# Kernel tuning notes

Measured on AMD Instinct MI355X. Metric: run time of the kernel, lower is better.

Reference implementation:

```python
import jax, jax.numpy as jnp
import numpy as np

B, N, E = 4, 50000, 800000
C_IN, C_OUT, EF, EH = 64, 64, 10, 4  # heads=1, concat=False


def setup_inputs() -> dict:
    key = jax.random.key(0)
    ks = jax.random.split(key, 11)
    x = jax.random.normal(ks[0], (B, N, C_IN), jnp.float32)
    edge_index = jax.random.randint(ks[1], (2, E), 0, N, jnp.int32)
    edge_attr = jax.random.normal(ks[2], (E, EF), jnp.float32)
    # edge MLP params (both Linear layers bias=False)
    W1 = jax.random.normal(ks[3], (EF, EH), jnp.float32) / np.sqrt(EF)
    W2 = jax.random.normal(ks[4], (EH, EH), jnp.float32) / np.sqrt(EH)
    # GATConv params (heads=1): shared lin for src/dst, edge lin, attention vectors, bias
    W = jax.random.normal(ks[5], (C_IN, C_OUT), jnp.float32) / np.sqrt(C_IN)
    lin_edge_W = jax.random.normal(ks[6], (EH, C_OUT), jnp.float32) / np.sqrt(EH)
    att_src = jax.random.normal(ks[7], (C_OUT,), jnp.float32) / np.sqrt(C_OUT)
    att_dst = jax.random.normal(ks[8], (C_OUT,), jnp.float32) / np.sqrt(C_OUT)
    att_edge = jax.random.normal(ks[9], (C_OUT,), jnp.float32) / np.sqrt(C_OUT)
    bias = jnp.zeros((C_OUT,), jnp.float32)
    return {"x": x, "edge_index": edge_index, "edge_attr": edge_attr,
            "W1": W1, "W2": W2, "W": W, "lin_edge_W": lin_edge_W,
            "att_src": att_src, "att_dst": att_dst, "att_edge": att_edge,
            "bias": bias}


def reference(x, edge_index, edge_attr, W1, W2, W, lin_edge_W,
              att_src, att_dst, att_edge, bias):
    # edge MLP (LeakyReLU default slope 0.01), batch-independent
    e = jax.nn.leaky_relu(edge_attr @ W1, 0.01) @ W2            # [E, EH]
    src, dst = edge_index[0], edge_index[1]
    # PyG GATConv default add_self_loops=True, fill_value='mean':
    # self-loop edge attr = mean of incoming edge attrs per dst node
    cnt = jax.ops.segment_sum(jnp.ones((E,), e.dtype), dst, num_segments=N)
    loop_attr = jax.ops.segment_sum(e, dst, num_segments=N) / jnp.maximum(cnt, 1.0)[:, None]
    e_full = jnp.concatenate([e, loop_attr], axis=0)            # [E+N, EH]
    ar = jnp.arange(N, dtype=src.dtype)
    src_f = jnp.concatenate([src, ar])
    dst_f = jnp.concatenate([dst, ar])
    # edge attention logit contribution (batch-independent)
    a_edge = (e_full @ lin_edge_W) @ att_edge                   # [E+N]

    def per_batch(xb):
        h = xb @ W                                              # [N, C_OUT]
        a_s = h @ att_src                                       # [N]
        a_d = h @ att_dst                                       # [N]
        logits = jax.nn.leaky_relu(a_s[src_f] + a_d[dst_f] + a_edge, 0.2)
        # segment softmax over incoming edges of each dst node
        m = jax.ops.segment_max(logits, dst_f, num_segments=N)
        ex = jnp.exp(logits - m[dst_f])
        denom = jax.ops.segment_sum(ex, dst_f, num_segments=N)
        alpha = ex / denom[dst_f]                               # [E+N]
        out = jax.ops.segment_sum(h[src_f] * alpha[:, None], dst_f, num_segments=N)
        return jax.nn.elu(out + bias)                           # [N, C_OUT]

    # vectorizes the original Python loop over the batch dim
    return jax.vmap(per_batch)(x)  # dropout p=0.5 is identity in eval mode
```

## Files before the change

kernel.cpp:

```cpp
#include <hip/hip_runtime.h>
#include <math.h>

#define NN 50000
#define NE 800000
#define NB 4
#define C  64
#define EF 10
#define EH 4

__device__ __forceinline__ float lrelu(float x, float s) { return x > 0.f ? x : s * x; }

__device__ __forceinline__ unsigned int f2bf(float f) {
    unsigned u = __float_as_uint(f);
    u += 0x7FFF + ((u >> 16) & 1);
    return u >> 16;
}

__global__ void __launch_bounds__(256) fused_prep_kernel(
        const float* __restrict__ x, const float* __restrict__ W,
        const float* __restrict__ att_src, const float* __restrict__ att_dst,
        unsigned* __restrict__ hbf, float* __restrict__ a_s, float* __restrict__ a_d,
        const float* __restrict__ edge_attr, const int* __restrict__ edge_index,
        const float* __restrict__ W1, const float* __restrict__ W2,
        const float* __restrict__ linW, const float* __restrict__ attE,
        int* __restrict__ cnt, int* __restrict__ rank, float* __restrict__ aE) {
    __shared__ float Wl[C * C];
    __shared__ float xT[C * 64];
    __shared__ float u4s[EH];
    int t = threadIdx.x;
    int bid = blockIdx.x;

    if ((bid & 1) == 0) {
        if (t < 64) {
            float av = attE[t];
            float vv[EH];
#pragma unroll
            for (int h = 0; h < EH; h++) {
                float p = linW[h * C + t] * av;
#pragma unroll
                for (int off = 32; off; off >>= 1) p += __shfl_xor(p, off);
                vv[h] = p;
            }
            if (t < EH) {
                float s = 0.f;
#pragma unroll
                for (int h = 0; h < EH; h++) s += W2[t * EH + h] * vv[h];
                u4s[t] = s;
            }
        }
        int e = (bid >> 1) * 256 + t;
        int d = edge_index[NE + e];
        rank[e] = atomicAdd(&cnt[d], 1);
        const float* ea = edge_attr + (size_t)e * EF;
        float s0 = 0.f, s1 = 0.f, s2 = 0.f, s3 = 0.f;
#pragma unroll
        for (int f = 0; f < EF; f++) {
            float ev = ea[f];
            s0 += ev * W1[f * EH + 0];
            s1 += ev * W1[f * EH + 1];
            s2 += ev * W1[f * EH + 2];
            s3 += ev * W1[f * EH + 3];
        }
        __syncthreads();
        aE[e] = lrelu(s0, 0.01f) * u4s[0] + lrelu(s1, 0.01f) * u4s[1] +
                lrelu(s2, 0.01f) * u4s[2] + lrelu(s3, 0.01f) * u4s[3];
        return;
    }

    for (int i = t * 4; i < C * C; i += 256 * 4)
        *(float4*)&Wl[i] = *(const float4*)&W[i];
    size_t row0 = (size_t)(bid >> 1) * 64;
    int r = t >> 2;
    int k0 = (t & 3) * 16;
    const float4* xr = (const float4*)(x + (row0 + r) * C + k0);
    float4 v0 = xr[0], v1 = xr[1], v2 = xr[2], v3 = xr[3];
    xT[(k0 + 0) * 64 + r] = v0.x;  xT[(k0 + 1) * 64 + r] = v0.y;
    xT[(k0 + 2) * 64 + r] = v0.z;  xT[(k0 + 3) * 64 + r] = v0.w;
    xT[(k0 + 4) * 64 + r] = v1.x;  xT[(k0 + 5) * 64 + r] = v1.y;
    xT[(k0 + 6) * 64 + r] = v1.z;  xT[(k0 + 7) * 64 + r] = v1.w;
    xT[(k0 + 8) * 64 + r] = v2.x;  xT[(k0 + 9) * 64 + r] = v2.y;
    xT[(k0 + 10) * 64 + r] = v2.z; xT[(k0 + 11) * 64 + r] = v2.w;
    xT[(k0 + 12) * 64 + r] = v3.x; xT[(k0 + 13) * 64 + r] = v3.y;
    xT[(k0 + 14) * 64 + r] = v3.z; xT[(k0 + 15) * 64 + r] = v3.w;
    __syncthreads();

    int col4 = (t & 15) * 4;
    int row4 = (t >> 4) * 4;
    float acc[4][4];
#pragma unroll
    for (int i = 0; i < 4; i++)
#pragma unroll
        for (int j = 0; j < 4; j++) acc[i][j] = 0.f;

#pragma unroll 8
    for (int k = 0; k < C; k++) {
        float4 wv = *(float4*)&Wl[k * C + col4];
        float4 xv = *(float4*)&xT[k * 64 + row4];
        const float xs[4] = {xv.x, xv.y, xv.z, xv.w};
        const float ws[4] = {wv.x, wv.y, wv.z, wv.w};
#pragma unroll
        for (int i = 0; i < 4; i++)
#pragma unroll
            for (int j = 0; j < 4; j++) acc[i][j] += xs[i] * ws[j];
    }

#pragma unroll
    for (int i = 0; i < 4; i++) {
        size_t gr = row0 + row4 + i;
        int b = (int)(gr / NN);
        int n = (int)(gr - (size_t)b * NN);
        uint2 p;
        p.x = f2bf(acc[i][0]) | (f2bf(acc[i][1]) << 16);
        p.y = f2bf(acc[i][2]) | (f2bf(acc[i][3]) << 16);
        *(uint2*)&hbf[((size_t)n * NB + b) * (C / 2) + (col4 >> 1)] = p;
    }
    float4 sa = *(const float4*)&att_src[col4];
    float4 da = *(const float4*)&att_dst[col4];
#pragma unroll
    for (int i = 0; i < 4; i++) {
        float ps = acc[i][0] * sa.x + acc[i][1] * sa.y + acc[i][2] * sa.z + acc[i][3] * sa.w;
        float pd = acc[i][0] * da.x + acc[i][1] * da.y + acc[i][2] * da.z + acc[i][3] * da.w;
#pragma unroll
        for (int off = 8; off; off >>= 1) {
            ps += __shfl_xor(ps, off);
            pd += __shfl_xor(pd, off);
        }
        if ((t & 15) == 0) {
            a_s[row0 + row4 + i] = ps;
            a_d[row0 + row4 + i] = pd;
        }
    }
}

__global__ void scan_block_kernel(const int* __restrict__ cnt, int* __restrict__ rowptr,
                                  int* __restrict__ bsum) {
    __shared__ int sh[1024];
    int i = blockIdx.x * 1024 + threadIdx.x;
    sh[threadIdx.x] = (i < NN) ? cnt[i] : 0;
    __syncthreads();
    for (int off = 1; off < 1024; off <<= 1) {
        int t = (threadIdx.x >= (unsigned)off) ? sh[threadIdx.x - off] : 0;
        __syncthreads();
        sh[threadIdx.x] += t;
        __syncthreads();
    }
    if (i < NN) rowptr[1 + i] = sh[threadIdx.x];
    if (threadIdx.x == 1023) bsum[blockIdx.x] = sh[1023];
}

__global__ void scan_add_kernel(int* __restrict__ rowptr, const int* __restrict__ bsum) {
    __shared__ int sbase;
    int bid = blockIdx.x;
    if (threadIdx.x < 64) {
        int v = (threadIdx.x < bid) ? bsum[threadIdx.x] : 0;
#pragma unroll
        for (int off = 32; off; off >>= 1) v += __shfl_xor(v, off);
        if (threadIdx.x == 0) sbase = v;
    }
    __syncthreads();
    int i = bid * 1024 + threadIdx.x;
    if (i < NN) rowptr[1 + i] += sbase;
    if (i == 0) rowptr[0] = 0;
}

__global__ void scatter_kernel(const int* __restrict__ edge_index,
                               const int* __restrict__ rowptr,
                               const int* __restrict__ rank,
                               const float* __restrict__ aE,
                               uint2* __restrict__ csr) {
    int g0 = blockIdx.x * blockDim.x + threadIdx.x;
    if (g0 >= NE / 4) return;
#pragma unroll
    for (int q = 0; q < 4; q++) {
        int e = g0 + q * (NE / 4);
        int s = edge_index[e];
        int d = edge_index[NE + e];
        int idx = rowptr[d] + rank[e];
        uint2 p;
        p.x = (unsigned)s;
        p.y = __float_as_uint(aE[e]);
        csr[idx] = p;
    }
}

__global__ void gather_kernel(const int* __restrict__ rowptr, const uint2* __restrict__ csr,
                              const float* __restrict__ a_s, const float* __restrict__ a_d,
                              const uint2* __restrict__ hbf,
                              const float* __restrict__ bias, float* __restrict__ out) {
    int n = blockIdx.x * (blockDim.x >> 6) + (threadIdx.x >> 6);
    if (n >= NN) return;
    int lane = threadIdx.x & 63;
    int b = lane >> 4;
    int t = lane & 15;
    int r0 = rowptr[n];
    int deg = rowptr[n + 1] - r0;
    const float* asb = a_s + (size_t)b * NN;
    float adst = a_d[(size_t)b * NN + n];

    float ds = 0.f;
    float aEs = 0.f;
    float4 acc = make_float4(0.f, 0.f, 0.f, 0.f);
    for (int base = 0; base < deg; base += 16) {
        int j = base + t;
        float ex = 0.f;
        int sreg = 0;
        if (j < deg) {
            uint2 pr = csr[r0 + j];
            sreg = (int)pr.x;
            float aev = __uint_as_float(pr.y);
            aEs += aev;
            ex = __expf(lrelu(asb[sreg] + adst + aev, 0.2f));
        }
        ds += ex;
        int cn = min(16, deg - base);
        for (int jo = 0; jo < cn; jo += 8) {
            float al[8];
            uint2 hv[8];
#pragma unroll
            for (int k2 = 0; k2 < 8; k2++) {
                int j2 = jo + k2;
                int sl = (b << 4) + (j2 & 15);
                float av = __shfl(ex, sl);
                int sj = __shfl(sreg, sl);
                al[k2] = (j2 < cn) ? av : 0.f;
                hv[k2] = hbf[(size_t)sj * (NB * C / 4) + (b << 4) + t];
            }
#pragma unroll
            for (int k2 = 0; k2 < 8; k2++) {
                acc.x += al[k2] * __uint_as_float(hv[k2].x << 16);
                acc.y += al[k2] * __uint_as_float(hv[k2].x & 0xFFFF0000u);
                acc.z += al[k2] * __uint_as_float(hv[k2].y << 16);
                acc.w += al[k2] * __uint_as_float(hv[k2].y & 0xFFFF0000u);
            }
        }
    }
#pragma unroll
    for (int off = 8; off; off >>= 1) {
        ds += __shfl_xor(ds, off);
        aEs += __shfl_xor(aEs, off);
    }
    float a_loop = aEs / fmaxf((float)deg, 1.0f);
    float eloop = __expf(lrelu(asb[n] + adst + a_loop, 0.2f));
    float inv = 1.f / (ds + eloop);
    uint2 hv = hbf[(size_t)n * (NB * C / 4) + (b << 4) + t];
    float4 bv = ((const float4*)bias)[t];
    float4 o;
    o.x = (acc.x + eloop * __uint_as_float(hv.x << 16)) * inv + bv.x;
    o.y = (acc.y + eloop * __uint_as_float(hv.x & 0xFFFF0000u)) * inv + bv.y;
    o.z = (acc.z + eloop * __uint_as_float(hv.y << 16)) * inv + bv.z;
    o.w = (acc.w + eloop * __uint_as_float(hv.y & 0xFFFF0000u)) * inv + bv.w;
    o.x = o.x > 0.f ? o.x : __expf(o.x) - 1.f;
    o.y = o.y > 0.f ? o.y : __expf(o.y) - 1.f;
    o.z = o.z > 0.f ? o.z : __expf(o.z) - 1.f;
    o.w = o.w > 0.f ? o.w : __expf(o.w) - 1.f;
    ((float4*)out)[((size_t)b * NN + n) * 16 + t] = o;
}

extern "C" void kernel_launch(void* const* d_in, const int* in_sizes, int n_in,
                              void* d_out, int out_size, void* d_ws, size_t ws_size,
                              hipStream_t stream) {
    const float* x      = (const float*)d_in[0];
    const int* eidx     = (const int*)d_in[1];
    const float* eattr  = (const float*)d_in[2];
    const float* W1     = (const float*)d_in[3];
    const float* W2     = (const float*)d_in[4];
    const float* W      = (const float*)d_in[5];
    const float* linW   = (const float*)d_in[6];
    const float* attS   = (const float*)d_in[7];
    const float* attD   = (const float*)d_in[8];
    const float* attE   = (const float*)d_in[9];
    const float* bias   = (const float*)d_in[10];
    float* out = (float*)d_out;

    size_t off = 0;
    auto alloc = [&](size_t bytes) {
        void* p = (char*)d_ws + off;
        off += (bytes + 255) / 256 * 256;
        return p;
    };
    int* cnt      = (int*)alloc((size_t)NN * 4);
    int* rowptr   = (int*)alloc((size_t)(NN + 1) * 4);
    int* bsum     = (int*)alloc(64 * 4);
    int* rank     = (int*)alloc((size_t)NE * 4);
    float* aE     = (float*)alloc((size_t)NE * 4);
    uint2* csr    = (uint2*)alloc((size_t)NE * 8);
    unsigned* hbf = (unsigned*)alloc((size_t)NN * NB * C * 2);
    float* a_s    = (float*)alloc((size_t)NB * NN * 4);
    float* a_d    = (float*)alloc((size_t)NB * NN * 4);
    (void)ws_size; (void)n_in; (void)in_sizes; (void)out_size;

    hipMemsetAsync(cnt, 0, (size_t)NN * 4, stream);

    fused_prep_kernel<<<6250, 256, 0, stream>>>(x, W, attS, attD, hbf, a_s, a_d,
                                                eattr, eidx, W1, W2, linW, attE,
                                                cnt, rank, aE);

    int nblk = (NN + 1023) / 1024;
    scan_block_kernel<<<nblk, 1024, 0, stream>>>(cnt, rowptr, bsum);
    scan_add_kernel<<<nblk, 1024, 0, stream>>>(rowptr, bsum);

    scatter_kernel<<<(NE / 4 + 255) / 256, 256, 0, stream>>>(eidx, rowptr, rank, aE, csr);

    gather_kernel<<<(NN + 3) / 4, 256, 0, stream>>>(rowptr, csr, a_s, a_d,
                                                    (const uint2*)hbf, bias, out);
}
```

Before: 150.7 us.

## Move degree counting first and fuse edge MLP with CSR scatter

The atomic degree/rank counting moves into a small standalone kernel that runs before the prefix scan. The edge-MLP computation then happens inside the fused GEMM kernel after the scan, so each edge writes its (src, attention) pair straight to its CSR slot. This removes the separate scatter kernel and the aE intermediate buffer round trip. In exchange the edge index is read twice and there is one extra launch for the degree pass.

```diff
diff --git a/kernel.cpp b/kernel.cpp
--- a/kernel.cpp
+++ b/kernel.cpp
@@ -16,14 +16,52 @@
     return u >> 16;
 }
 
-__global__ void __launch_bounds__(256) fused_prep_kernel(
+__global__ void degree_kernel(const int* __restrict__ edge_index, int* __restrict__ cnt,
+                              int* __restrict__ rank) {
+    int e = blockIdx.x * blockDim.x + threadIdx.x;
+    if (e < NE) rank[e] = atomicAdd(&cnt[edge_index[NE + e]], 1);
+}
+
+__global__ void scan_block_kernel(const int* __restrict__ cnt, int* __restrict__ rowptr,
+                                  int* __restrict__ bsum) {
+    __shared__ int sh[1024];
+    int i = blockIdx.x * 1024 + threadIdx.x;
+    sh[threadIdx.x] = (i < NN) ? cnt[i] : 0;
+    __syncthreads();
+    for (int off = 1; off < 1024; off <<= 1) {
+        int t = (threadIdx.x >= (unsigned)off) ? sh[threadIdx.x - off] : 0;
+        __syncthreads();
+        sh[threadIdx.x] += t;
+        __syncthreads();
+    }
+    if (i < NN) rowptr[1 + i] = sh[threadIdx.x];
+    if (threadIdx.x == 1023) bsum[blockIdx.x] = sh[1023];
+}
+
+__global__ void scan_add_kernel(int* __restrict__ rowptr, const int* __restrict__ bsum) {
+    __shared__ int sbase;
+    int bid = blockIdx.x;
+    if (threadIdx.x < 64) {
+        int v = (threadIdx.x < bid) ? bsum[threadIdx.x] : 0;
+#pragma unroll
+        for (int off = 32; off; off >>= 1) v += __shfl_xor(v, off);
+        if (threadIdx.x == 0) sbase = v;
+    }
+    __syncthreads();
+    int i = bid * 1024 + threadIdx.x;
+    if (i < NN) rowptr[1 + i] += sbase;
+    if (i == 0) rowptr[0] = 0;
+}
+
+__global__ void __launch_bounds__(256) fused_mlp_scatter_gemm_kernel(
         const float* __restrict__ x, const float* __restrict__ W,
         const float* __restrict__ att_src, const float* __restrict__ att_dst,
         unsigned* __restrict__ hbf, float* __restrict__ a_s, float* __restrict__ a_d,
         const float* __restrict__ edge_attr, const int* __restrict__ edge_index,
         const float* __restrict__ W1, const float* __restrict__ W2,
         const float* __restrict__ linW, const float* __restrict__ attE,
-        int* __restrict__ cnt, int* __restrict__ rank, float* __restrict__ aE) {
+        const int* __restrict__ rowptr, const int* __restrict__ rank,
+        uint2* __restrict__ csr) {
     __shared__ float Wl[C * C];
     __shared__ float xT[C * 64];
     __shared__ float u4s[EH];
@@ -49,8 +87,9 @@
             }
         }
         int e = (bid >> 1) * 256 + t;
+        int s = edge_index[e];
         int d = edge_index[NE + e];
-        rank[e] = atomicAdd(&cnt[d], 1);
+        int idx = rowptr[d] + rank[e];
         const float* ea = edge_attr + (size_t)e * EF;
         float s0 = 0.f, s1 = 0.f, s2 = 0.f, s3 = 0.f;
 #pragma unroll
@@ -62,8 +101,12 @@
             s3 += ev * W1[f * EH + 3];
         }
         __syncthreads();
-        aE[e] = lrelu(s0, 0.01f) * u4s[0] + lrelu(s1, 0.01f) * u4s[1] +
-                lrelu(s2, 0.01f) * u4s[2] + lrelu(s3, 0.01f) * u4s[3];
+        float a = lrelu(s0, 0.01f) * u4s[0] + lrelu(s1, 0.01f) * u4s[1] +
+                  lrelu(s2, 0.01f) * u4s[2] + lrelu(s3, 0.01f) * u4s[3];
+        uint2 p;
+        p.x = (unsigned)s;
+        p.y = __float_as_uint(a);
+        csr[idx] = p;
         return;
     }
 
@@ -132,57 +175,6 @@
     }
 }
 
-__global__ void scan_block_kernel(const int* __restrict__ cnt, int* __restrict__ rowptr,
-                                  int* __restrict__ bsum) {
-    __shared__ int sh[1024];
-    int i = blockIdx.x * 1024 + threadIdx.x;
-    sh[threadIdx.x] = (i < NN) ? cnt[i] : 0;
-    __syncthreads();
-    for (int off = 1; off < 1024; off <<= 1) {
-        int t = (threadIdx.x >= (unsigned)off) ? sh[threadIdx.x - off] : 0;
-        __syncthreads();
-        sh[threadIdx.x] += t;
-        __syncthreads();
-    }
-    if (i < NN) rowptr[1 + i] = sh[threadIdx.x];
-    if (threadIdx.x == 1023) bsum[blockIdx.x] = sh[1023];
-}
-
-__global__ void scan_add_kernel(int* __restrict__ rowptr, const int* __restrict__ bsum) {
-    __shared__ int sbase;
-    int bid = blockIdx.x;
-    if (threadIdx.x < 64) {
-        int v = (threadIdx.x < bid) ? bsum[threadIdx.x] : 0;
-#pragma unroll
-        for (int off = 32; off; off >>= 1) v += __shfl_xor(v, off);
-        if (threadIdx.x == 0) sbase = v;
-    }
-    __syncthreads();
-    int i = bid * 1024 + threadIdx.x;
-    if (i < NN) rowptr[1 + i] += sbase;
-    if (i == 0) rowptr[0] = 0;
-}
-
-__global__ void scatter_kernel(const int* __restrict__ edge_index,
-                               const int* __restrict__ rowptr,
-                               const int* __restrict__ rank,
-                               const float* __restrict__ aE,
-                               uint2* __restrict__ csr) {
-    int g0 = blockIdx.x * blockDim.x + threadIdx.x;
-    if (g0 >= NE / 4) return;
-#pragma unroll
-    for (int q = 0; q < 4; q++) {
-        int e = g0 + q * (NE / 4);
-        int s = edge_index[e];
-        int d = edge_index[NE + e];
-        int idx = rowptr[d] + rank[e];
-        uint2 p;
-        p.x = (unsigned)s;
-        p.y = __float_as_uint(aE[e]);
-        csr[idx] = p;
-    }
-}
-
 __global__ void gather_kernel(const int* __restrict__ rowptr, const uint2* __restrict__ csr,
                               const float* __restrict__ a_s, const float* __restrict__ a_d,
                               const uint2* __restrict__ hbf,
@@ -282,7 +274,6 @@
     int* rowptr   = (int*)alloc((size_t)(NN + 1) * 4);
     int* bsum     = (int*)alloc(64 * 4);
     int* rank     = (int*)alloc((size_t)NE * 4);
-    float* aE     = (float*)alloc((size_t)NE * 4);
     uint2* csr    = (uint2*)alloc((size_t)NE * 8);
     unsigned* hbf = (unsigned*)alloc((size_t)NN * NB * C * 2);
     float* a_s    = (float*)alloc((size_t)NB * NN * 4);
@@ -291,15 +282,15 @@
 
     hipMemsetAsync(cnt, 0, (size_t)NN * 4, stream);
 
-    fused_prep_kernel<<<6250, 256, 0, stream>>>(x, W, attS, attD, hbf, a_s, a_d,
-                                                eattr, eidx, W1, W2, linW, attE,
-                                                cnt, rank, aE);
+    degree_kernel<<<(NE + 255) / 256, 256, 0, stream>>>(eidx, cnt, rank);
 
     int nblk = (NN + 1023) / 1024;
     scan_block_kernel<<<nblk, 1024, 0, stream>>>(cnt, rowptr, bsum);
     scan_add_kernel<<<nblk, 1024, 0, stream>>>(rowptr, bsum);
 
-    scatter_kernel<<<(NE / 4 + 255) / 256, 256, 0, stream>>>(eidx, rowptr, rank, aE, csr);
+    fused_mlp_scatter_gemm_kernel<<<6250, 256, 0, stream>>>(
+        x, W, attS, attD, hbf, a_s, a_d,
+        eattr, eidx, W1, W2, linW, attE, rowptr, rank, csr);
 
     gather_kernel<<<(NN + 3) / 4, 256, 0, stream>>>(rowptr, csr, a_s, a_d,
                                                     (const uint2*)hbf, bias, out);
```

New measurement: 171.8 us. 1.14x slower.
